# Kernel optimization log

Measured on AMD Instinct MI355X. Metric: run time of the kernel, lower is better.

The kernel has to match this reference:

```python
import jax, jax.numpy as jnp
import numpy as np


def quat_to_rot(q):
    """kornia-style quaternion (x, y, z, w) -> rotation matrix, with normalization."""
    q = q / jnp.linalg.norm(q, axis=-1, keepdims=True)
    x, y, z, w = q[..., 0], q[..., 1], q[..., 2], q[..., 3]
    xx, yy, zz = x * x, y * y, z * z
    xy, xz, yz = x * y, x * z, y * z
    wx, wy, wz = w * x, w * y, w * z
    r = jnp.stack([
        jnp.stack([1.0 - 2.0 * (yy + zz), 2.0 * (xy - wz), 2.0 * (xz + wy)], axis=-1),
        jnp.stack([2.0 * (xy + wz), 1.0 - 2.0 * (xx + zz), 2.0 * (yz - wx)], axis=-1),
        jnp.stack([2.0 * (xz - wy), 2.0 * (yz + wx), 1.0 - 2.0 * (xx + yy)], axis=-1),
    ], axis=-2)  # [B, 3, 3]
    return r


def setup_inputs() -> dict:
    key = jax.random.key(0)
    k1, k2, k3 = jax.random.split(key, 3)
    B, N = 32, 262144
    return {
        "predquat": jax.random.normal(k1, (B, 4), dtype=jnp.float32),
        "gtquat": jax.random.normal(k2, (B, 4), dtype=jnp.float32),
        "points": jax.random.normal(k3, (B, 3, N), dtype=jnp.float32),
    }


def reference(predquat, gtquat, points):
    predrot = quat_to_rot(predquat)            # [B,3,3]
    gtrot = quat_to_rot(gtquat)                # [B,3,3]
    predpts = jnp.einsum('bij,bjn->bin', predrot, points)  # [B,3,N]
    gtpts = jnp.einsum('bij,bjn->bin', gtrot, points)      # [B,3,N]
    # PointCloudDistance(x=gtpts, y=predpts), exactly as the torch code:
    # x_y[b,i,j,n] = x[b,j,n] - y[b,i,n]; sum over n -> [B,3,3]
    diff = gtpts[:, None, :, :] - predpts[:, :, None, :]   # [B,3,3,N]
    d = jnp.sum(diff * diff, axis=3)                       # [B,3,3]
    row = jnp.min(d, axis=1)                               # min over i -> [B,3]
    chamfer = jnp.mean(jnp.mean(row, axis=1))
    return chamfer
```

## Files before the change

kernel.cpp:

```cpp
#include <hip/hip_runtime.h>

#define BPB 64
#define TPB 256

__global__ __launch_bounds__(TPB) void moments_kernel(
        const float* __restrict__ points, float* __restrict__ partials, int N) {
    const int b = blockIdx.y;
    const int n4 = N >> 2;
    const float4* __restrict__ px = (const float4*)(points + (size_t)b * 3 * N);
    const float4* __restrict__ py = px + n4;
    const float4* __restrict__ pz = px + 2 * n4;

    float sxx = 0.f, syy = 0.f, szz = 0.f, sxy = 0.f, sxz = 0.f, syz = 0.f;
    const int stride = BPB * TPB;
    #pragma unroll 2
    for (int i = blockIdx.x * TPB + threadIdx.x; i < n4; i += stride) {
        float4 x = px[i];
        float4 y = py[i];
        float4 z = pz[i];
        sxx += x.x * x.x + x.y * x.y + x.z * x.z + x.w * x.w;
        syy += y.x * y.x + y.y * y.y + y.z * y.z + y.w * y.w;
        szz += z.x * z.x + z.y * z.y + z.z * z.z + z.w * z.w;
        sxy += x.x * y.x + x.y * y.y + x.z * y.z + x.w * y.w;
        sxz += x.x * z.x + x.y * z.y + x.z * z.z + x.w * z.w;
        syz += y.x * z.x + y.y * z.y + y.z * z.z + y.w * z.w;
    }

    for (int off = 32; off > 0; off >>= 1) {
        sxx += __shfl_down(sxx, off);
        syy += __shfl_down(syy, off);
        szz += __shfl_down(szz, off);
        sxy += __shfl_down(sxy, off);
        sxz += __shfl_down(sxz, off);
        syz += __shfl_down(syz, off);
    }

    __shared__ float red[TPB / 64][6];
    const int wave = threadIdx.x >> 6;
    const int lane = threadIdx.x & 63;
    if (lane == 0) {
        red[wave][0] = sxx; red[wave][1] = syy; red[wave][2] = szz;
        red[wave][3] = sxy; red[wave][4] = sxz; red[wave][5] = syz;
    }
    __syncthreads();
    if (threadIdx.x < 6) {
        float s = 0.f;
        for (int w = 0; w < TPB / 64; ++w) s += red[w][threadIdx.x];
        partials[((size_t)b * BPB + blockIdx.x) * 6 + threadIdx.x] = s;
    }
}

__device__ inline void quat_to_rot_dev(float x, float y, float z, float w, float R[3][3]) {
    float inv = rsqrtf(x * x + y * y + z * z + w * w);
    x *= inv; y *= inv; z *= inv; w *= inv;
    const float xx = x * x, yy = y * y, zz = z * z;
    const float xy = x * y, xz = x * z, yz = y * z;
    const float wx = w * x, wy = w * y, wz = w * z;
    R[0][0] = 1.f - 2.f * (yy + zz); R[0][1] = 2.f * (xy - wz);       R[0][2] = 2.f * (xz + wy);
    R[1][0] = 2.f * (xy + wz);       R[1][1] = 1.f - 2.f * (xx + zz); R[1][2] = 2.f * (yz - wx);
    R[2][0] = 2.f * (xz - wy);       R[2][1] = 2.f * (yz + wx);       R[2][2] = 1.f - 2.f * (xx + yy);
}

__global__ __launch_bounds__(256) void finalize_kernel(
        const float* __restrict__ predquat,
        const float* __restrict__ gtquat,
        const float* __restrict__ partials,
        float* __restrict__ out, int B) {
    __shared__ float smom[32][6];
    const int t = threadIdx.x;
    if (t < B * 6) {
        const int bb = t / 6, k = t % 6;
        float s = 0.f;
        #pragma unroll 8
        for (int j = 0; j < BPB; ++j)
            s += partials[((size_t)bb * BPB + j) * 6 + k];
        smom[bb][k] = s;
    }
    __syncthreads();
    if (t >= 64) return;

    float val = 0.f;
    if (t < B) {
        const float* m = smom[t];
        const float M[3][3] = {{m[0], m[3], m[4]},
                               {m[3], m[1], m[5]},
                               {m[4], m[5], m[2]}};
        float P[3][3], G[3][3];
        quat_to_rot_dev(predquat[4 * t], predquat[4 * t + 1], predquat[4 * t + 2], predquat[4 * t + 3], P);
        quat_to_rot_dev(gtquat[4 * t], gtquat[4 * t + 1], gtquat[4 * t + 2], gtquat[4 * t + 3], G);

        float gg[3];
        for (int j = 0; j < 3; ++j) {
            const float t0 = G[j][0] * M[0][0] + G[j][1] * M[1][0] + G[j][2] * M[2][0];
            const float t1 = G[j][0] * M[0][1] + G[j][1] * M[1][1] + G[j][2] * M[2][1];
            const float t2 = G[j][0] * M[0][2] + G[j][1] * M[1][2] + G[j][2] * M[2][2];
            gg[j] = t0 * G[j][0] + t1 * G[j][1] + t2 * G[j][2];
        }
        float pp[3], cr[3][3];
        for (int i = 0; i < 3; ++i) {
            const float t0 = P[i][0] * M[0][0] + P[i][1] * M[1][0] + P[i][2] * M[2][0];
            const float t1 = P[i][0] * M[0][1] + P[i][1] * M[1][1] + P[i][2] * M[2][1];
            const float t2 = P[i][0] * M[0][2] + P[i][1] * M[1][2] + P[i][2] * M[2][2];
            pp[i] = t0 * P[i][0] + t1 * P[i][1] + t2 * P[i][2];
            for (int j = 0; j < 3; ++j)
                cr[i][j] = t0 * G[j][0] + t1 * G[j][1] + t2 * G[j][2];
        }
        float acc = 0.f;
        for (int j = 0; j < 3; ++j) {
            const float d0 = gg[j] + pp[0] - 2.f * cr[0][j];
            const float d1 = gg[j] + pp[1] - 2.f * cr[1][j];
            const float d2 = gg[j] + pp[2] - 2.f * cr[2][j];
            acc += fminf(d0, fminf(d1, d2));
        }
        val = acc / 3.f;
    }
    for (int off = 32; off > 0; off >>= 1) val += __shfl_down(val, off);
    if (t == 0) out[0] = val / (float)B;
}

extern "C" void kernel_launch(void* const* d_in, const int* in_sizes, int n_in,
                              void* d_out, int out_size, void* d_ws, size_t ws_size,
                              hipStream_t stream) {
    const float* predquat = (const float*)d_in[0];
    const float* gtquat   = (const float*)d_in[1];
    const float* points   = (const float*)d_in[2];
    float* out = (float*)d_out;
    float* partials = (float*)d_ws;

    const int B = in_sizes[0] / 4;
    const int N = in_sizes[2] / (B * 3);

    dim3 grid(BPB, B);
    moments_kernel<<<grid, TPB, 0, stream>>>(points, partials, N);
    finalize_kernel<<<1, 256, 0, stream>>>(predquat, gtquat, partials, out, B);
}
```

Before: 26.34 us.

## Fully unroll moments loop with nontemporal loads, fewer blocks, transposed partials

```diff
diff --git a/kernel.cpp b/kernel.cpp
--- a/kernel.cpp
+++ b/kernel.cpp
@@ -1,29 +1,50 @@
 #include <hip/hip_runtime.h>
 
-#define BPB 64
+#define BPB 32
 #define TPB 256
 
+typedef float vf4 __attribute__((ext_vector_type(4)));
+
+
+template <int ITERS>
 __global__ __launch_bounds__(TPB) void moments_kernel(
         const float* __restrict__ points, float* __restrict__ partials, int N) {
     const int b = blockIdx.y;
     const int n4 = N >> 2;
-    const float4* __restrict__ px = (const float4*)(points + (size_t)b * 3 * N);
-    const float4* __restrict__ py = px + n4;
-    const float4* __restrict__ pz = px + 2 * n4;
+    const vf4* __restrict__ px = (const vf4*)(points + (size_t)b * 3 * N);
+    const vf4* __restrict__ py = px + n4;
+    const vf4* __restrict__ pz = px + 2 * n4;
 
     float sxx = 0.f, syy = 0.f, szz = 0.f, sxy = 0.f, sxz = 0.f, syz = 0.f;
+    const int base = blockIdx.x * TPB + threadIdx.x;
     const int stride = BPB * TPB;
-    #pragma unroll 2
-    for (int i = blockIdx.x * TPB + threadIdx.x; i < n4; i += stride) {
-        float4 x = px[i];
-        float4 y = py[i];
-        float4 z = pz[i];
-        sxx += x.x * x.x + x.y * x.y + x.z * x.z + x.w * x.w;
-        syy += y.x * y.x + y.y * y.y + y.z * y.z + y.w * y.w;
-        szz += z.x * z.x + z.y * z.y + z.z * z.z + z.w * z.w;
-        sxy += x.x * y.x + x.y * y.y + x.z * y.z + x.w * y.w;
-        sxz += x.x * z.x + x.y * z.y + x.z * z.z + x.w * z.w;
-        syz += y.x * z.x + y.y * z.y + y.z * z.z + y.w * z.w;
+
+    if constexpr (ITERS > 0) {
+        #pragma unroll
+        for (int it = 0; it < ITERS; ++it) {
+            const int i = base + it * stride;
+            const vf4 x = __builtin_nontemporal_load(&px[i]);
+            const vf4 y = __builtin_nontemporal_load(&py[i]);
+            const vf4 z = __builtin_nontemporal_load(&pz[i]);
+            sxx += x.x * x.x + x.y * x.y + x.z * x.z + x.w * x.w;
+            syy += y.x * y.x + y.y * y.y + y.z * y.z + y.w * y.w;
+            szz += z.x * z.x + z.y * z.y + z.z * z.z + z.w * z.w;
+            sxy += x.x * y.x + x.y * y.y + x.z * y.z + x.w * y.w;
+            sxz += x.x * z.x + x.y * z.y + x.z * z.z + x.w * z.w;
+            syz += y.x * z.x + y.y * z.y + y.z * z.z + y.w * z.w;
+        }
+    } else {
+        for (int i = base; i < n4; i += stride) {
+            const vf4 x = px[i];
+            const vf4 y = py[i];
+            const vf4 z = pz[i];
+            sxx += x.x * x.x + x.y * x.y + x.z * x.z + x.w * x.w;
+            syy += y.x * y.x + y.y * y.y + y.z * y.z + y.w * y.w;
+            szz += z.x * z.x + z.y * z.y + z.z * z.z + z.w * z.w;
+            sxy += x.x * y.x + x.y * y.y + x.z * y.z + x.w * y.w;
+            sxz += x.x * z.x + x.y * z.y + x.z * z.z + x.w * z.w;
+            syz += y.x * z.x + y.y * z.y + y.z * z.z + y.w * z.w;
+        }
     }
 
     for (int off = 32; off > 0; off >>= 1) {
@@ -46,7 +67,7 @@
     if (threadIdx.x < 6) {
         float s = 0.f;
         for (int w = 0; w < TPB / 64; ++w) s += red[w][threadIdx.x];
-        partials[((size_t)b * BPB + blockIdx.x) * 6 + threadIdx.x] = s;
+        partials[((size_t)b * 6 + threadIdx.x) * BPB + blockIdx.x] = s;
     }
 }
 
@@ -70,10 +91,13 @@
     const int t = threadIdx.x;
     if (t < B * 6) {
         const int bb = t / 6, k = t % 6;
+        const vf4* p = (const vf4*)&partials[((size_t)bb * 6 + k) * BPB];
         float s = 0.f;
-        #pragma unroll 8
-        for (int j = 0; j < BPB; ++j)
-            s += partials[((size_t)bb * BPB + j) * 6 + k];
+        #pragma unroll
+        for (int j = 0; j < BPB / 4; ++j) {
+            const vf4 v = p[j];
+            s += v.x + v.y + v.z + v.w;
+        }
         smom[bb][k] = s;
     }
     __syncthreads();
@@ -131,6 +155,12 @@
     const int N = in_sizes[2] / (B * 3);
 
     dim3 grid(BPB, B);
-    moments_kernel<<<grid, TPB, 0, stream>>>(points, partials, N);
+    const int n4 = N >> 2;
+    const int stride = BPB * TPB;
+    if (n4 == 8 * stride) {
+        moments_kernel<8><<<grid, TPB, 0, stream>>>(points, partials, N);
+    } else {
+        moments_kernel<0><<<grid, TPB, 0, stream>>>(points, partials, N);
+    }
     finalize_kernel<<<1, 256, 0, stream>>>(predquat, gtquat, partials, out, B);
 }
```

Result: faster. 21.64 us, median of 2 (-17.8%).
